# Kernel optimization log

Measured on AMD Instinct MI355X. Metric: run time of the kernel, lower is better.

## Reference

```python
import jax, jax.numpy as jnp
import numpy as np

EPS = 1e-12

def l2norm(x):
    # torch F.normalize(p=2, dim=-1): x / max(||x||, eps)
    n = jnp.sqrt(jnp.sum(x * x, axis=-1, keepdims=True))
    return x / jnp.maximum(n, EPS)

def grid_sample_zeros(img, grid):
    """Bilinear grid_sample, padding_mode='zeros', align_corners=False.
    img: [B,C,H,W], grid: [B,P,2] with (x,y) in [-1,1]. Returns [B,C,P]."""
    B, C, H, W = img.shape
    ix = ((grid[..., 0] + 1.0) * W - 1.0) * 0.5  # [B,P]
    iy = ((grid[..., 1] + 1.0) * H - 1.0) * 0.5
    x0 = jnp.floor(ix); x1 = x0 + 1.0
    y0 = jnp.floor(iy); y1 = y0 + 1.0
    wx1 = ix - x0; wx0 = 1.0 - wx1
    wy1 = iy - y0; wy0 = 1.0 - wy1

    def gather(xf, yf):
        valid = ((xf >= 0) & (xf <= W - 1) & (yf >= 0) & (yf <= H - 1)).astype(img.dtype)
        xi = jnp.clip(xf, 0, W - 1).astype(jnp.int32)
        yi = jnp.clip(yf, 0, H - 1).astype(jnp.int32)
        v = jax.vmap(lambda im, yy, xx: im[:, yy, xx])(img, yi, xi)  # [B,C,P]
        return v * valid[:, None, :]

    out = (gather(x0, y0) * (wx0 * wy0)[:, None, :]
         + gather(x1, y0) * (wx1 * wy0)[:, None, :]
         + gather(x0, y1) * (wx0 * wy1)[:, None, :]
         + gather(x1, y1) * (wx1 * wy1)[:, None, :])
    return out


def setup_inputs() -> dict:
    key = jax.random.key(0)
    ks = jax.random.split(key, 8)
    B, N, K, C = 4, 512, 128, 256
    H8 = W8 = 128
    H16 = W16 = 64
    inp = {
        'node_reliability_weights': jax.random.normal(ks[0], (B, N), jnp.float32),
        'node_features': jax.random.normal(ks[1], (B, N, C), jnp.float32),
        'rel_map_8': jax.random.normal(ks[2], (B, H8, W8), jnp.float32),
        'feat_map_8': jax.random.normal(ks[3], (B, C, H8, W8), jnp.float32),
        'rel_map_16': jax.random.normal(ks[4], (B, H16, W16), jnp.float32),
        'feat_map_16': jax.random.normal(ks[5], (B, C, H16, W16), jnp.float32),
        # normalized coords in [-1,1]
        'coords': jax.random.uniform(ks[6], (B, K, N, 2), jnp.float32) * 2.0 - 1.0,
        'logit_scale': jnp.asarray(np.log(1.0 / 0.07), jnp.float32),
    }
    return inp


def reference(node_reliability_weights, node_features, rel_map_8, feat_map_8,
              rel_map_16, feat_map_16, coords, logit_scale):
    B, N, C = node_features.shape
    K = coords.shape[1]
    nnf = l2norm(node_features)  # [B,N,C]
    # [B,K,N,2] -> [B,N,K,2] -> [B,N*K,2]
    grid = jnp.transpose(coords, (0, 2, 1, 3)).reshape(B, N * K, 2)

    sims, rels = [], []
    for rel_map, feat_map in ((rel_map_8, feat_map_8), (rel_map_16, feat_map_16)):
        sr = grid_sample_zeros(rel_map[:, None], grid).reshape(B, N, K)
        sf = grid_sample_zeros(feat_map, grid).reshape(B, C, N, K)
        nsf = l2norm(jnp.transpose(sf, (0, 2, 3, 1)))  # [B,N,K,C]
        sims.append(jnp.einsum('bnc,bnkc->bnk', nnf, nsf))
        rels.append(node_reliability_weights[:, :, None] + sr)

    S = len(sims)
    total_sim = jnp.stack(sims, axis=-1)  # [B,N,K,S]
    total_rel = jnp.stack(rels, axis=-1)  # [B,N,K,S]
    total_rel = jnp.transpose(total_rel, (0, 2, 1, 3)).reshape(B, K, N * S)
    total_rel = jax.nn.softmax(total_rel, axis=-1)
    total_sim = jnp.transpose(total_sim, (0, 2, 1, 3)).reshape(B, K, N * S)
    logits = jnp.sum(total_sim * total_rel, axis=-1) * jnp.exp(logit_scale)  # [B,K]
    return jax.nn.softmax(logits, axis=1)
```

## Files before the change

kernel.cpp:

```cpp
#include <hip/hip_runtime.h>
#include <math.h>

typedef _Float16 f16;
typedef _Float16 f16x2 __attribute__((ext_vector_type(2)));
typedef _Float16 f16x4 __attribute__((ext_vector_type(4)));

namespace {
constexpr int B = 4, N = 512, K = 128, C = 256;
constexpr int H8 = 128, W8 = 128, P8 = H8 * W8;
constexpr int H16 = 64, W16 = 64, P16 = H16 * W16;
constexpr int NB = 16;
constexpr int NBINS = B * NB;
constexpr int NSAMP = B * K * N;
constexpr int CAP = 4608;
constexpr int SLOTS = NBINS * CAP;
constexpr int NWGS = SLOTS / 32;
}

__device__ __forceinline__ float fdot2a(f16x2 a, f16x2 b, float c)
{
#if __has_builtin(__builtin_amdgcn_fdot2)
    return __builtin_amdgcn_fdot2(a, b, c, false);
#else
    return c + (float)a.x * (float)b.x + (float)a.y * (float)b.y;
#endif
}

__device__ __forceinline__ float red16_sum(float x)
{
    int t;
    t = __builtin_amdgcn_update_dpp(0, __float_as_int(x), 0xB1,  0xF, 0xF, true);
    x += __int_as_float(t);
    t = __builtin_amdgcn_update_dpp(0, __float_as_int(x), 0x4E,  0xF, 0xF, true);
    x += __int_as_float(t);
    t = __builtin_amdgcn_update_dpp(0, __float_as_int(x), 0x141, 0xF, 0xF, true);
    x += __int_as_float(t);
    t = __builtin_amdgcn_update_dpp(0, __float_as_int(x), 0x140, 0xF, 0xF, true);
    x += __int_as_float(t);
    return x;
}

__device__ __forceinline__ int band_of(float gy)
{
    int band = (int)((gy + 1.0f) * 0.5f * NB);
    return min(NB - 1, max(0, band));
}

__global__ __launch_bounds__(256) void k_transpose(
    const float* __restrict__ in, f16* __restrict__ out, int P)
{
    __shared__ float tile[64][65];
    const int b  = blockIdx.z;
    const int p0 = blockIdx.x * 64;
    const int c0 = blockIdx.y * 64;
    const int tid = threadIdx.x;
    const int tp = tid & 63, tq = tid >> 6;
    const float* src = in + (size_t)b * C * P;
    f16* dst = out + (size_t)b * P * C;
#pragma unroll
    for (int i = 0; i < 16; ++i) {
        const int cl = tq + i * 4;
        tile[cl][tp] = src[(size_t)(c0 + cl) * P + (p0 + tp)];
    }
    __syncthreads();
#pragma unroll
    for (int i = 0; i < 16; ++i) {
        const int pl = tq + i * 4;
        dst[(size_t)(p0 + pl) * C + (c0 + tp)] = (f16)tile[tp][pl];
    }
}

__global__ __launch_bounds__(256) void k_prenorm(
    const float* __restrict__ nodef, f16* __restrict__ nnf)
{
    const int node = blockIdx.x * 4 + (threadIdx.x >> 6);
    const int lane = threadIdx.x & 63;
    const float4 v = *reinterpret_cast<const float4*>(
        nodef + (size_t)node * C + lane * 4);
    float nn = v.x * v.x + v.y * v.y + v.z * v.z + v.w * v.w;
#pragma unroll
    for (int off = 32; off; off >>= 1) nn += __shfl_xor(nn, off);
    const float inv = __frsqrt_rn(fmaxf(nn, 1e-24f));
    f16x4 o;
    o.x = (f16)(v.x * inv); o.y = (f16)(v.y * inv);
    o.z = (f16)(v.z * inv); o.w = (f16)(v.w * inv);
    *reinterpret_cast<f16x4*>(nnf + (size_t)node * C + lane * 4) = o;
}

__global__ __launch_bounds__(256) void k_scatter(
    const float* __restrict__ coords, unsigned* __restrict__ cursor,
    unsigned* __restrict__ order)
{
    __shared__ unsigned cnt[NBINS], base[NBINS];
    const int tid = threadIdx.x;
    const int sid0 = blockIdx.x * 512;

    if (tid < NBINS) cnt[tid] = 0;
    __syncthreads();

    int bin[2];
#pragma unroll
    for (int j = 0; j < 2; ++j) {
        const int sid = sid0 + j * 256 + tid;
        const float gy = coords[(size_t)sid * 2 + 1];
        bin[j] = (sid >> 16) * NB + band_of(gy);
        atomicAdd(&cnt[bin[j]], 1u);
    }
    __syncthreads();
    if (tid < NBINS) {
        base[tid] = cnt[tid] ? atomicAdd(&cursor[tid], cnt[tid]) : 0u;
    }
    __syncthreads();
    if (tid < NBINS) cnt[tid] = 0;
    __syncthreads();
#pragma unroll
    for (int j = 0; j < 2; ++j) {
        const int sid = sid0 + j * 256 + tid;
        const unsigned rank = atomicAdd(&cnt[bin[j]], 1u);
        const unsigned r = base[bin[j]] + rank;
        if (r < CAP) order[(size_t)bin[j] * CAP + r] = (unsigned)sid;
    }
}

__global__ __launch_bounds__(256) void k_sample(
    const float* __restrict__ nodew,
    const f16*  __restrict__ nnf,
    const float* __restrict__ rel8,
    const float* __restrict__ rel16,
    const float* __restrict__ coords,
    const f16*  __restrict__ ft8,
    const f16*  __restrict__ ft16,
    const unsigned* __restrict__ order,
    float4* __restrict__ sr)
{
    const int data = ((blockIdx.x & 7) * (NWGS / 8)) + (blockIdx.x >> 3);
    const int tid = threadIdx.x;
    const int grp = tid >> 4, gl = tid & 15, cg = gl * 16;
    const int slot0 = data * 32 + grp * 2;

    unsigned sid[2];
    sid[0] = order[slot0];
    sid[1] = order[slot0 + 1];

    bool val[2];
    int bb[2], kv[2], nv[2];
    float gx[2], gy[2], wr[2];
    f16x2 nf2[2][8];
#pragma unroll
    for (int j = 0; j < 2; ++j) {
        val[j] = (sid[j] != 0xFFFFFFFFu);
        const unsigned s = val[j] ? sid[j] : 0u;
        nv[j] = s & 511; kv[j] = (s >> 9) & 127; bb[j] = (int)(s >> 16);
        gx[j] = coords[(size_t)s * 2 + 0];
        gy[j] = coords[(size_t)s * 2 + 1];
        wr[j] = nodew[bb[j] * N + nv[j]];
        const f16* np_ = nnf + ((size_t)(bb[j] * N + nv[j])) * C + cg;
        float4 r0 = *reinterpret_cast<const float4*>(np_);
        float4 r1 = *reinterpret_cast<const float4*>(np_ + 8);
        const f16x2* h0 = reinterpret_cast<const f16x2*>(&r0);
        const f16x2* h1 = reinterpret_cast<const f16x2*>(&r1);
#pragma unroll
        for (int c = 0; c < 4; ++c) { nf2[j][c] = h0[c]; nf2[j][c + 4] = h1[c]; }
    }

    int   pp[4][4];
    f16x2 ww[4][4];
    float srv[4];
    const f16* fb[4];
#pragma unroll
    for (int ph = 0; ph < 4; ++ph) {
        const int j = ph >> 1, s = ph & 1;
        const int W_ = s ? W16 : W8;
        const int H_ = s ? H16 : H8;
        const float* __restrict__ relm =
            (s ? rel16 : rel8) + (size_t)bb[j] * (s ? P16 : P8);
        fb[ph] = (s ? ft16 : ft8) + (size_t)bb[j] * (s ? P16 : P8) * C;

        const float ix = ((gx[j] + 1.0f) * W_ - 1.0f) * 0.5f;
        const float iy = ((gy[j] + 1.0f) * H_ - 1.0f) * 0.5f;
        const float x0f = floorf(ix), y0f = floorf(iy);
        const int x0 = (int)x0f, y0 = (int)y0f;
        const int x1 = x0 + 1, y1 = y0 + 1;
        const float fx1 = ix - x0f, fx0 = 1.0f - fx1;
        const float fy1 = iy - y0f, fy0 = 1.0f - fy1;
        const bool vx0 = (x0 >= 0) && (x0 < W_);
        const bool vx1 = (x1 >= 0) && (x1 < W_);
        const bool vy0 = (y0 >= 0) && (y0 < H_);
        const bool vy1 = (y1 >= 0) && (y1 < H_);
        float w[4];
        w[0] = (vx0 && vy0) ? fx0 * fy0 : 0.0f;
        w[1] = (vx1 && vy0) ? fx1 * fy0 : 0.0f;
        w[2] = (vx0 && vy1) ? fx0 * fy1 : 0.0f;
        w[3] = (vx1 && vy1) ? fx1 * fy1 : 0.0f;
        const int cx0 = min(max(x0, 0), W_ - 1);
        const int cx1 = min(max(x1, 0), W_ - 1);
        const int cy0 = min(max(y0, 0), H_ - 1);
        const int cy1 = min(max(y1, 0), H_ - 1);
        pp[ph][0] = cy0 * W_ + cx0; pp[ph][1] = cy0 * W_ + cx1;
        pp[ph][2] = cy1 * W_ + cx0; pp[ph][3] = cy1 * W_ + cx1;
        srv[ph] = w[0] * relm[pp[ph][0]] + w[1] * relm[pp[ph][1]]
                + w[2] * relm[pp[ph][2]] + w[3] * relm[pp[ph][3]];
#pragma unroll
        for (int t = 0; t < 4; ++t) {
            const f16 h = (f16)w[t];
            ww[ph][t] = f16x2{h, h};
        }
    }

    float4 ra[2][4], rb[2][4];
#pragma unroll
    for (int t = 0; t < 4; ++t) {
        const f16* tp = fb[0] + (size_t)pp[0][t] * C + cg;
        ra[0][t] = *reinterpret_cast<const float4*>(tp);
        rb[0][t] = *reinterpret_cast<const float4*>(tp + 8);
    }

    float simv[4];
#pragma unroll
    for (int ph = 0; ph < 4; ++ph) {
        const int cur = ph & 1, nxt = cur ^ 1;
        if (ph < 3) {
#pragma unroll
            for (int t = 0; t < 4; ++t) {
                const f16* tp = fb[ph + 1] + (size_t)pp[ph + 1][t] * C + cg;
                ra[nxt][t] = *reinterpret_cast<const float4*>(tp);
                rb[nxt][t] = *reinterpret_cast<const float4*>(tp + 8);
            }
        }

        f16x2 v[8];
        {
            const f16x2* a0 = reinterpret_cast<const f16x2*>(&ra[cur][0]);
            const f16x2* b0 = reinterpret_cast<const f16x2*>(&rb[cur][0]);
#pragma unroll
            for (int c = 0; c < 4; ++c) {
                v[c]     = ww[ph][0] * a0[c];
                v[c + 4] = ww[ph][0] * b0[c];
            }
        }
#pragma unroll
        for (int t = 1; t < 4; ++t) {
            const f16x2* at = reinterpret_cast<const f16x2*>(&ra[cur][t]);
            const f16x2* bt = reinterpret_cast<const f16x2*>(&rb[cur][t]);
#pragma unroll
            for (int c = 0; c < 4; ++c) {
                v[c]     += ww[ph][t] * at[c];
                v[c + 4] += ww[ph][t] * bt[c];
            }
        }

        float dot = 0.0f, n2 = 0.0f;
        const int j = ph >> 1;
#pragma unroll
        for (int c = 0; c < 8; ++c) {
            dot = fdot2a(nf2[j][c], v[c], dot);
            n2  = fdot2a(v[c], v[c], n2);
        }
        dot = red16_sum(dot);
        n2  = red16_sum(n2);
        simv[ph] = dot * __frsqrt_rn(fmaxf(n2, 1e-24f));
    }

#pragma unroll
    for (int j = 0; j < 2; ++j) {
        if (val[j] && gl == 0) {
            sr[(size_t)(bb[j] * K + kv[j]) * N + nv[j]] =
                make_float4(simv[j * 2], simv[j * 2 + 1],
                            wr[j] + srv[j * 2], wr[j] + srv[j * 2 + 1]);
        }
    }
}

__global__ __launch_bounds__(256) void k_logits(
    const float4* __restrict__ sr, const float* __restrict__ lscale,
    float* __restrict__ logits)
{
    const int bk = blockIdx.x;
    const int tid = threadIdx.x;
    const int lane = tid & 63, wid = tid >> 6;
    const float4* sp = sr + (size_t)bk * N;
    __shared__ float red0[4], red1[4], red2[4];

    float4 e0 = sp[tid], e1 = sp[tid + 256];
    float m = fmaxf(fmaxf(e0.z, e0.w), fmaxf(e1.z, e1.w));
#pragma unroll
    for (int off = 32; off; off >>= 1) m = fmaxf(m, __shfl_xor(m, off));
    if (lane == 0) red0[wid] = m;
    __syncthreads();
    m = fmaxf(fmaxf(red0[0], red0[1]), fmaxf(red0[2], red0[3]));

    const float a0 = expf(e0.z - m), a1 = expf(e0.w - m);
    const float b0 = expf(e1.z - m), b1 = expf(e1.w - m);
    float se = a0 + a1 + b0 + b1;
    float ss = a0 * e0.x + a1 * e0.y + b0 * e1.x + b1 * e1.y;
#pragma unroll
    for (int off = 32; off; off >>= 1) {
        se += __shfl_xor(se, off);
        ss += __shfl_xor(ss, off);
    }
    if (lane == 0) { red1[wid] = se; red2[wid] = ss; }
    __syncthreads();
    if (tid == 0) {
        const float tse = red1[0] + red1[1] + red1[2] + red1[3];
        const float tss = red2[0] + red2[1] + red2[2] + red2[3];
        logits[bk] = (tss / tse) * expf(lscale[0]);
    }
}

__global__ __launch_bounds__(64) void k_out(
    const float* __restrict__ logits, float* __restrict__ out)
{
    const int b = blockIdx.x;
    const int lane = threadIdx.x;
    const float v0 = logits[b * K + lane];
    const float v1 = logits[b * K + lane + 64];
    float m = fmaxf(v0, v1);
#pragma unroll
    for (int off = 32; off; off >>= 1) m = fmaxf(m, __shfl_xor(m, off));
    const float e0 = expf(v0 - m), e1 = expf(v1 - m);
    float se = e0 + e1;
#pragma unroll
    for (int off = 32; off; off >>= 1) se += __shfl_xor(se, off);
    out[b * K + lane] = e0 / se;
    out[b * K + lane + 64] = e1 / se;
}

extern "C" void kernel_launch(void* const* d_in, const int* in_sizes, int n_in,
                              void* d_out, int out_size, void* d_ws, size_t ws_size,
                              hipStream_t stream)
{
    const float* nodew  = (const float*)d_in[0];
    const float* nodef  = (const float*)d_in[1];
    const float* rel8   = (const float*)d_in[2];
    const float* feat8  = (const float*)d_in[3];
    const float* rel16  = (const float*)d_in[4];
    const float* feat16 = (const float*)d_in[5];
    const float* coords = (const float*)d_in[6];
    const float* lscale = (const float*)d_in[7];

    char* ws = (char*)d_ws;
    size_t off = 0;
    f16* ft8  = (f16*)(ws + off); off += (size_t)B * P8 * C * 2;
    f16* ft16 = (f16*)(ws + off); off += (size_t)B * P16 * C * 2;
    f16* nnf  = (f16*)(ws + off); off += (size_t)B * N * C * 2;
    float4* sr = (float4*)(ws + off); off += (size_t)NSAMP * 16;
    float* logits = (float*)(ws + off); off += (size_t)B * K * 4;
    unsigned* order  = (unsigned*)(ws + off); off += (size_t)SLOTS * 4;
    unsigned* cursor = (unsigned*)(ws + off); off += NBINS * 4;
    float* out = (float*)d_out;

    hipMemsetAsync(order, 0xFF, (size_t)SLOTS * sizeof(unsigned), stream);
    hipMemsetAsync(cursor, 0, NBINS * sizeof(unsigned), stream);

    hipLaunchKernelGGL(k_transpose, dim3(P8 / 64, C / 64, B), dim3(256), 0, stream,
                       feat8, ft8, P8);
    hipLaunchKernelGGL(k_transpose, dim3(P16 / 64, C / 64, B), dim3(256), 0, stream,
                       feat16, ft16, P16);
    hipLaunchKernelGGL(k_prenorm, dim3(B * N / 4), dim3(256), 0, stream,
                       nodef, nnf);
    hipLaunchKernelGGL(k_scatter, dim3(NSAMP / 512), dim3(256), 0, stream,
                       coords, cursor, order);
    hipLaunchKernelGGL(k_sample, dim3(NWGS), dim3(256), 0, stream,
                       nodew, nnf, rel8, rel16, coords, ft8, ft16, order, sr);
    hipLaunchKernelGGL(k_logits, dim3(B * K), dim3(256), 0, stream,
                       sr, lscale, logits);
    hipLaunchKernelGGL(k_out, dim3(B), dim3(64), 0, stream, logits, out);
}
```

Before: 105.0 us.

## Sort samples into dense 2D spatial bins via count, scan and scatter

Replaces the fixed-capacity 1D row-band bucketing with a 32x32 2D spatial histogram per batch. A count kernel and a single-block prefix scan give exact offsets, so the order array is dense with no padding slots, invalid entries or capacity overflow. The sampling kernel drops its validity checks and changes the per-thread work mapping so each sample's two scales are processed in a different order. The goal is better cache locality for the bilinear gathers and no wasted padded workgroups, at the cost of two extra kernel launches and more shared-memory atomics in the binning kernels.

```diff
diff --git a/kernel.cpp b/kernel.cpp
--- a/kernel.cpp
+++ b/kernel.cpp
@@ -9,12 +9,11 @@
 constexpr int B = 4, N = 512, K = 128, C = 256;
 constexpr int H8 = 128, W8 = 128, P8 = H8 * W8;
 constexpr int H16 = 64, W16 = 64, P16 = H16 * W16;
-constexpr int NB = 16;
-constexpr int NBINS = B * NB;
+constexpr int NBG = 32;
+constexpr int LBINS = NBG * NBG;
+constexpr int NBINS = B * LBINS;
 constexpr int NSAMP = B * K * N;
-constexpr int CAP = 4608;
-constexpr int SLOTS = NBINS * CAP;
-constexpr int NWGS = SLOTS / 32;
+constexpr int NWGS = NSAMP / 32;
 }
 
 __device__ __forceinline__ float fdot2a(f16x2 a, f16x2 b, float c)
@@ -40,10 +39,10 @@
     return x;
 }
 
-__device__ __forceinline__ int band_of(float gy)
-{
-    int band = (int)((gy + 1.0f) * 0.5f * NB);
-    return min(NB - 1, max(0, band));
+__device__ __forceinline__ int band32(float g)
+{
+    int v = (int)((g + 1.0f) * 0.5f * NBG);
+    return min(NBG - 1, max(0, v));
 }
 
 __global__ __launch_bounds__(256) void k_transpose(
@@ -87,38 +86,79 @@
     *reinterpret_cast<f16x4*>(nnf + (size_t)node * C + lane * 4) = o;
 }
 
+__global__ __launch_bounds__(256) void k_count(
+    const float* __restrict__ coords, unsigned* __restrict__ hist)
+{
+    __shared__ unsigned cnt[LBINS];
+    const int tid = threadIdx.x;
+    const int sid0 = blockIdx.x * 512;
+    const int b = sid0 >> 16;
+    for (int i = tid; i < LBINS; i += 256) cnt[i] = 0;
+    __syncthreads();
+#pragma unroll
+    for (int j = 0; j < 2; ++j) {
+        const int sid = sid0 + j * 256 + tid;
+        const float gx = coords[(size_t)sid * 2 + 0];
+        const float gy = coords[(size_t)sid * 2 + 1];
+        atomicAdd(&cnt[band32(gy) * NBG + band32(gx)], 1u);
+    }
+    __syncthreads();
+    for (int i = tid; i < LBINS; i += 256)
+        if (cnt[i]) atomicAdd(&hist[b * LBINS + i], cnt[i]);
+}
+
+__global__ __launch_bounds__(256) void k_scan(
+    const unsigned* __restrict__ hist, unsigned* __restrict__ cursor)
+{
+    __shared__ unsigned sums[256];
+    const int t = threadIdx.x;
+    unsigned v[16];
+    unsigned s = 0;
+#pragma unroll
+    for (int i = 0; i < 16; ++i) { v[i] = s; s += hist[t * 16 + i]; }
+    sums[t] = s;
+    __syncthreads();
+    for (int off = 1; off < 256; off <<= 1) {
+        const unsigned x = (t >= off) ? sums[t - off] : 0u;
+        __syncthreads();
+        sums[t] += x;
+        __syncthreads();
+    }
+    const unsigned pre = (t == 0) ? 0u : sums[t - 1];
+#pragma unroll
+    for (int i = 0; i < 16; ++i) cursor[t * 16 + i] = pre + v[i];
+}
+
 __global__ __launch_bounds__(256) void k_scatter(
     const float* __restrict__ coords, unsigned* __restrict__ cursor,
     unsigned* __restrict__ order)
 {
-    __shared__ unsigned cnt[NBINS], base[NBINS];
+    __shared__ unsigned cnt[LBINS], base[LBINS];
     const int tid = threadIdx.x;
     const int sid0 = blockIdx.x * 512;
-
-    if (tid < NBINS) cnt[tid] = 0;
-    __syncthreads();
-
-    int bin[2];
+    const int b = sid0 >> 16;
+    for (int i = tid; i < LBINS; i += 256) cnt[i] = 0;
+    __syncthreads();
+    int bl[2];
 #pragma unroll
     for (int j = 0; j < 2; ++j) {
         const int sid = sid0 + j * 256 + tid;
+        const float gx = coords[(size_t)sid * 2 + 0];
         const float gy = coords[(size_t)sid * 2 + 1];
-        bin[j] = (sid >> 16) * NB + band_of(gy);
-        atomicAdd(&cnt[bin[j]], 1u);
-    }
-    __syncthreads();
-    if (tid < NBINS) {
-        base[tid] = cnt[tid] ? atomicAdd(&cursor[tid], cnt[tid]) : 0u;
-    }
-    __syncthreads();
-    if (tid < NBINS) cnt[tid] = 0;
+        bl[j] = band32(gy) * NBG + band32(gx);
+        atomicAdd(&cnt[bl[j]], 1u);
+    }
+    __syncthreads();
+    for (int i = tid; i < LBINS; i += 256)
+        base[i] = cnt[i] ? atomicAdd(&cursor[b * LBINS + i], cnt[i]) : 0u;
+    __syncthreads();
+    for (int i = tid; i < LBINS; i += 256) cnt[i] = 0;
     __syncthreads();
 #pragma unroll
     for (int j = 0; j < 2; ++j) {
         const int sid = sid0 + j * 256 + tid;
-        const unsigned rank = atomicAdd(&cnt[bin[j]], 1u);
-        const unsigned r = base[bin[j]] + rank;
-        if (r < CAP) order[(size_t)bin[j] * CAP + r] = (unsigned)sid;
+        const unsigned r = base[bl[j]] + atomicAdd(&cnt[bl[j]], 1u);
+        order[r] = (unsigned)sid;
     }
 }
 
@@ -142,14 +182,12 @@
     sid[0] = order[slot0];
     sid[1] = order[slot0 + 1];
 
-    bool val[2];
     int bb[2], kv[2], nv[2];
     float gx[2], gy[2], wr[2];
     f16x2 nf2[2][8];
 #pragma unroll
     for (int j = 0; j < 2; ++j) {
-        val[j] = (sid[j] != 0xFFFFFFFFu);
-        const unsigned s = val[j] ? sid[j] : 0u;
+        const unsigned s = sid[j];
         nv[j] = s & 511; kv[j] = (s >> 9) & 127; bb[j] = (int)(s >> 16);
         gx[j] = coords[(size_t)s * 2 + 0];
         gy[j] = coords[(size_t)s * 2 + 1];
@@ -169,7 +207,7 @@
     const f16* fb[4];
 #pragma unroll
     for (int ph = 0; ph < 4; ++ph) {
-        const int j = ph >> 1, s = ph & 1;
+        const int j = ph & 1, s = ph >> 1;
         const int W_ = s ? W16 : W8;
         const int H_ = s ? H16 : H8;
         const float* __restrict__ relm =
@@ -250,7 +288,7 @@
         }
 
         float dot = 0.0f, n2 = 0.0f;
-        const int j = ph >> 1;
+        const int j = ph & 1;
 #pragma unroll
         for (int c = 0; c < 8; ++c) {
             dot = fdot2a(nf2[j][c], v[c], dot);
@@ -261,12 +299,12 @@
         simv[ph] = dot * __frsqrt_rn(fmaxf(n2, 1e-24f));
     }
 
-#pragma unroll
-    for (int j = 0; j < 2; ++j) {
-        if (val[j] && gl == 0) {
+    if (gl == 0) {
+#pragma unroll
+        for (int j = 0; j < 2; ++j) {
             sr[(size_t)(bb[j] * K + kv[j]) * N + nv[j]] =
-                make_float4(simv[j * 2], simv[j * 2 + 1],
-                            wr[j] + srv[j * 2], wr[j] + srv[j * 2 + 1]);
+                make_float4(simv[j], simv[2 + j],
+                            wr[j] + srv[j], wr[j] + srv[2 + j]);
         }
     }
 }
@@ -345,12 +383,12 @@
     f16* nnf  = (f16*)(ws + off); off += (size_t)B * N * C * 2;
     float4* sr = (float4*)(ws + off); off += (size_t)NSAMP * 16;
     float* logits = (float*)(ws + off); off += (size_t)B * K * 4;
-    unsigned* order  = (unsigned*)(ws + off); off += (size_t)SLOTS * 4;
+    unsigned* order  = (unsigned*)(ws + off); off += (size_t)NSAMP * 4;
+    unsigned* hist   = (unsigned*)(ws + off); off += NBINS * 4;
     unsigned* cursor = (unsigned*)(ws + off); off += NBINS * 4;
     float* out = (float*)d_out;
 
-    hipMemsetAsync(order, 0xFF, (size_t)SLOTS * sizeof(unsigned), stream);
-    hipMemsetAsync(cursor, 0, NBINS * sizeof(unsigned), stream);
+    hipMemsetAsync(hist, 0, NBINS * sizeof(unsigned), stream);
 
     hipLaunchKernelGGL(k_transpose, dim3(P8 / 64, C / 64, B), dim3(256), 0, stream,
                        feat8, ft8, P8);
@@ -358,6 +396,9 @@
                        feat16, ft16, P16);
     hipLaunchKernelGGL(k_prenorm, dim3(B * N / 4), dim3(256), 0, stream,
                        nodef, nnf);
+    hipLaunchKernelGGL(k_count, dim3(NSAMP / 512), dim3(256), 0, stream,
+                       coords, hist);
+    hipLaunchKernelGGL(k_scan, dim3(1), dim3(256), 0, stream, hist, cursor);
     hipLaunchKernelGGL(k_scatter, dim3(NSAMP / 512), dim3(256), 0, stream,
                        coords, cursor, order);
     hipLaunchKernelGGL(k_sample, dim3(NWGS), dim3(256), 0, stream,
```

New measurement: 103.4 us. About the same (-1.5%).
